# Performance work log

Measured on AMD Instinct MI355X. Metric: run time of the kernel, lower is better.

The kernel has to match this reference:

```python
import jax, jax.numpy as jnp
import numpy as np

N = 50000
NUM_USERS = 20000
E = 800000
IN_DIM = 256
OUT_DIM = 256
H = 8
DK = OUT_DIM // H


def setup_inputs() -> dict:
    key = jax.random.key(0)
    ks = jax.random.split(key, 16)
    inp = {
        "x": jax.random.normal(ks[0], (N, IN_DIM), dtype=jnp.float32),
        "row": jax.random.randint(ks[1], (E,), 0, N, dtype=jnp.int32),
        "col": jax.random.randint(ks[2], (E,), 0, N, dtype=jnp.int32),
        "relation_emb": jax.random.normal(ks[3], (OUT_DIM,), dtype=jnp.float32),
        "user_text_embs": jax.random.normal(ks[4], (NUM_USERS, IN_DIM), dtype=jnp.float32),
        "item_text_embs": jax.random.normal(ks[5], (N - NUM_USERS, IN_DIM), dtype=jnp.float32),
        "Wq": jax.random.normal(ks[6], (OUT_DIM, IN_DIM), dtype=jnp.float32) * 0.02,
        "bq": jnp.zeros((OUT_DIM,), dtype=jnp.float32),
        "Wk": jax.random.normal(ks[7], (OUT_DIM, IN_DIM), dtype=jnp.float32) * 0.02,
        "bk": jnp.zeros((OUT_DIM,), dtype=jnp.float32),
        "Wv": jax.random.normal(ks[8], (OUT_DIM, IN_DIM), dtype=jnp.float32) * 0.02,
        "bv": jnp.zeros((OUT_DIM,), dtype=jnp.float32),
        "Wo": jax.random.normal(ks[9], (OUT_DIM, OUT_DIM), dtype=jnp.float32) * 0.02,
        "bo": jnp.zeros((OUT_DIM,), dtype=jnp.float32),
    }
    return inp


def reference(x, row, col, relation_emb, user_text_embs, item_text_embs,
              Wq, bq, Wk, bk, Wv, bv, Wo, bo):
    # text_emb: users first, then items (matches torch zeros_like + slice assign)
    text_emb = jnp.concatenate([user_text_embs, item_text_embs], axis=0)  # [N, in_dim]

    Q = (text_emb @ Wq.T + bq).reshape(N, H, DK)
    K = (text_emb @ Wk.T + bk).reshape(N, H, DK)
    V = (x @ Wv.T + bv).reshape(N, H, DK)

    Q_ = Q[col]  # [E, H, DK]
    K_ = K[row]
    V_ = V[row]
    rel = relation_emb.reshape(1, H, DK)

    scores = jnp.sum(Q_ * (K_ + rel), axis=-1) / np.sqrt(DK).astype(np.float32)  # [E, H]

    # segment softmax over destination node (col)
    m = jax.ops.segment_max(scores, col, num_segments=N)          # [N, H]
    e = jnp.exp(scores - m[col])                                   # [E, H]
    denom = jax.ops.segment_sum(e, col, num_segments=N)           # [N, H]
    attn = e / denom[col]                                          # [E, H]

    out = jax.ops.segment_sum(attn[:, :, None] * V_, col, num_segments=N)  # [N, H, DK]
    out = out.reshape(N, OUT_DIM)
    return out @ Wo.T + bo
```

## Files before the change

kernel.cpp:

```cpp
#include <hip/hip_runtime.h>
#include <hip/hip_bf16.h>

#define N_NODES   50000
#define N_USERS   20000
#define N_EDGES   800000
#define DIM       256
#define NHEAD     8
#define DKH       32
#define NBLK_SCAN ((N_NODES + 255) / 256)
#define NGRP      (N_NODES / 16)
#define NGRP_PAD  3128
#define SLOTS_NODE (NGRP * 8 * 64)
#define NBLK_CAST (SLOTS_NODE / 256)
#define NBLK_HIST ((N_EDGES + 255) / 256)
#define NBLK_G64  (NGRP_PAD / 4)
#define KVROW     768

typedef __attribute__((ext_vector_type(8))) short bf16x8;
typedef __attribute__((ext_vector_type(4))) float f32x4;
typedef __attribute__((ext_vector_type(4))) unsigned short u16x4;
typedef __attribute__((ext_vector_type(8))) unsigned short u16x8;

__device__ inline unsigned short f2bf(float f) {
    union { __hip_bfloat16 b; unsigned short u; } cv;
    cv.b = __float2bfloat16(f);
    return cv.u;
}
__device__ inline float bf2f(unsigned short u) {
    return __uint_as_float(((unsigned int)u) << 16);
}
__device__ inline unsigned char f2fp8(float f) {
    unsigned int p = __builtin_amdgcn_cvt_pk_fp8_f32(f, f, 0, false);
    return (unsigned char)(p & 0xff);
}


__global__ void prep_kernel(const float* __restrict__ Wq, const float* __restrict__ Wk,
                            const float* __restrict__ Wv, const float* __restrict__ Wo,
                            unsigned short* __restrict__ Wb2,
                            const float* __restrict__ x,
                            const float* __restrict__ user, const float* __restrict__ item,
                            unsigned short* __restrict__ xb2, unsigned short* __restrict__ tb2,
                            const int* __restrict__ col, int* __restrict__ cnt,
                            int* __restrict__ erank)
{
    int b = blockIdx.x;
    if (b < 128) {
        int gid = b * 256 + threadIdx.x;
        const float* srcs[4] = { Wq, Wk, Wv, Wo };
        int m = gid >> 13, slot = gid & 8191;
        int lane = slot & 63, ks = (slot >> 6) & 7, g = slot >> 9;
        int c = g * 16 + (lane & 15);
        int d = ks * 32 + (lane >> 4) * 8;
        const float* s = srcs[m] + (size_t)c * DIM + d;
        float4 f0 = *(const float4*)s, f1 = *(const float4*)(s + 4);
        u16x8 o = { f2bf(f0.x), f2bf(f0.y), f2bf(f0.z), f2bf(f0.w),
                    f2bf(f1.x), f2bf(f1.y), f2bf(f1.z), f2bf(f1.w) };
        *(u16x8*)(Wb2 + (size_t)m * 65536 + (size_t)slot * 8) = o;
    } else if (b < 128 + NBLK_CAST) {
        int slot = (b - 128) * 256 + threadIdx.x;
        int lane = slot & 63, ks = (slot >> 6) & 7, g = slot >> 9;
        int r = g * 16 + (lane & 15);
        int d = ks * 32 + (lane >> 4) * 8;

        const float* sx = x + (size_t)r * DIM + d;
        float4 f0 = *(const float4*)sx, f1 = *(const float4*)(sx + 4);
        u16x8 xo = { f2bf(f0.x), f2bf(f0.y), f2bf(f0.z), f2bf(f0.w),
                     f2bf(f1.x), f2bf(f1.y), f2bf(f1.z), f2bf(f1.w) };
        *(u16x8*)(xb2 + (size_t)slot * 8) = xo;

        const float* st = (r < N_USERS) ? user + (size_t)r * DIM + d
                                        : item + (size_t)(r - N_USERS) * DIM + d;
        float4 t0 = *(const float4*)st, t1 = *(const float4*)(st + 4);
        u16x8 to = { f2bf(t0.x), f2bf(t0.y), f2bf(t0.z), f2bf(t0.w),
                     f2bf(t1.x), f2bf(t1.y), f2bf(t1.z), f2bf(t1.w) };
        *(u16x8*)(tb2 + (size_t)slot * 8) = to;
    } else {
        int e = (b - 128 - NBLK_CAST) * 256 + threadIdx.x;
        if (e < N_EDGES) erank[e] = atomicAdd(&cnt[col[e]], 1);
    }
}

__device__ __forceinline__ void mfma_core64(const unsigned short* __restrict__ A2,
                                            const unsigned short* __restrict__ W2,
                                            int row0, f32x4 acc[2][8],
                                            int lane, int wid)
{
    const int gA = (row0 >> 4) + (wid >> 1) * 2;
    const int gB = (wid & 1) * 8;
    #pragma unroll
    for (int ks = 0; ks < 8; ++ks) {
        bf16x8 a[2], b[8];
        #pragma unroll
        for (int i = 0; i < 2; ++i)
            a[i] = *(const bf16x8*)(A2 + (size_t)((gA + i) * 8 + ks) * 512 + lane * 8);
        #pragma unroll
        for (int j = 0; j < 8; ++j)
            b[j] = *(const bf16x8*)(W2 + (size_t)((gB + j) * 8 + ks) * 512 + lane * 8);
        #pragma unroll
        for (int i = 0; i < 2; ++i)
            #pragma unroll
            for (int j = 0; j < 8; ++j)
                acc[i][j] = __builtin_amdgcn_mfma_f32_16x16x32_bf16(a[i], b[j], acc[i][j], 0, 0, 0);
    }
}

template<int MODE>
__device__ __forceinline__ void epilogue64(f32x4 acc[2][8], const float* bias, void* Cv,
                                           int row0, int M, int lane, int wid)
{
    const int wm = wid >> 1, wn = wid & 1;
    const int lr = lane & 15, lk = lane >> 4;
    float* Cf = (float*)Cv;
    unsigned short* Cb = (unsigned short*)Cv;
    unsigned char* C8 = (unsigned char*)Cv;
    #pragma unroll
    for (int i = 0; i < 2; ++i) {
        #pragma unroll
        for (int r = 0; r < 4; ++r) {
            int grow = row0 + wm * 32 + i * 16 + lk * 4 + r;
            if (grow >= M) continue;
            #pragma unroll
            for (int j = 0; j < 8; ++j) {
                int gcol = wn * 128 + j * 16 + lr;
                float val = acc[i][j][r] + bias[gcol];
                if constexpr (MODE == 0) {
                    Cf[(size_t)grow * 256 + gcol] = val;
                } else if constexpr (MODE == 1) {
                    Cb[(size_t)grow * 256 + gcol] = f2bf(val);
                } else if constexpr (MODE == 2) {
                    C8[(size_t)grow * KVROW + gcol] = f2fp8(val);
                } else {
                    *(unsigned short*)(C8 + (size_t)grow * KVROW + 256 + gcol * 2) = f2bf(val);
                }
            }
        }
    }
}

__global__ __launch_bounds__(256) void gemm_qkv_scatter(
    const unsigned short* __restrict__ tb2, const unsigned short* __restrict__ xb2,
    const unsigned short* __restrict__ Wb2,
    const float* __restrict__ bq, const float* __restrict__ bk, const float* __restrict__ bv,
    unsigned short* __restrict__ Qb, unsigned char* __restrict__ KVb, int M,
    const int* __restrict__ row, const int* __restrict__ col,
    const int* __restrict__ erank, const int* __restrict__ offs,
    int* __restrict__ esrc)
{
    const int b = blockIdx.x;
    if (b < NBLK_HIST) {
        int e = b * 256 + threadIdx.x;
        if (e < N_EDGES) {
            int c = col[e];
            esrc[offs[c] + erank[e]] = row[e];
        }
        return;
    }
    const int gb = b - NBLK_HIST;
    const int mat = gb / NBLK_G64;
    const int row0 = (gb % NBLK_G64) * 64;
    const int tid = threadIdx.x;
    const int lane = tid & 63, wid = tid >> 6;

    const unsigned short* A2 = (mat == 2) ? xb2 : tb2;
    const unsigned short* W2 = Wb2 + (size_t)mat * 65536;

    f32x4 acc[2][8];
    #pragma unroll
    for (int i = 0; i < 2; ++i)
        #pragma unroll
        for (int j = 0; j < 8; ++j) acc[i][j] = (f32x4){0.f, 0.f, 0.f, 0.f};

    mfma_core64(A2, W2, row0, acc, lane, wid);

    if (mat == 0)      epilogue64<1>(acc, bq, Qb,  row0, M, lane, wid);
    else if (mat == 1) epilogue64<2>(acc, bk, KVb, row0, M, lane, wid);
    else               epilogue64<3>(acc, bv, KVb, row0, M, lane, wid);
}

__global__ __launch_bounds__(256) void gemm_o_reg(
    const unsigned short* __restrict__ A2,
    const unsigned short* __restrict__ Wb2, const float* __restrict__ bo,
    float* __restrict__ C, int M)
{
    const int tid = threadIdx.x;
    const int lane = tid & 63, wid = tid >> 6;
    const int row0 = blockIdx.x * 64;

    f32x4 acc[2][8];
    #pragma unroll
    for (int i = 0; i < 2; ++i)
        #pragma unroll
        for (int j = 0; j < 8; ++j) acc[i][j] = (f32x4){0.f, 0.f, 0.f, 0.f};

    mfma_core64(A2, Wb2 + 3 * 65536, row0, acc, lane, wid);
    epilogue64<0>(acc, bo, C, row0, M, lane, wid);
}

__global__ __launch_bounds__(256) void scan_blk_kernel(const int* __restrict__ cnt,
                                                       int* __restrict__ offs_tmp,
                                                       int* __restrict__ bsum) {
    __shared__ int s[256];
    int b = blockIdx.x, t = threadIdx.x;
    int i = b * 256 + t;
    int v = (i < N_NODES) ? cnt[i] : 0;
    s[t] = v;
    __syncthreads();
    #pragma unroll
    for (int d = 1; d < 256; d <<= 1) {
        int u = (t >= d) ? s[t - d] : 0;
        __syncthreads();
        s[t] += u;
        __syncthreads();
    }
    if (i < N_NODES) offs_tmp[i] = s[t] - v;
    if (t == 255) bsum[b] = s[255];
}

__global__ __launch_bounds__(256) void scan_top_kernel(int* __restrict__ bsum) {
    __shared__ int s[256];
    int t = threadIdx.x;
    int v = (t < NBLK_SCAN) ? bsum[t] : 0;
    s[t] = v;
    __syncthreads();
    #pragma unroll
    for (int d = 1; d < 256; d <<= 1) {
        int u = (t >= d) ? s[t - d] : 0;
        __syncthreads();
        s[t] += u;
        __syncthreads();
    }
    if (t < NBLK_SCAN) bsum[t] = s[t] - v;
}

__global__ __launch_bounds__(256) void scan_add_kernel(const int* __restrict__ offs_tmp,
                                                       const int* __restrict__ bsum,
                                                       int* __restrict__ offs) {
    int i = blockIdx.x * 256 + threadIdx.x;
    if (i == 0) offs[N_NODES] = N_EDGES;
    if (i >= N_NODES) return;
    offs[i] = offs_tmp[i] + bsum[blockIdx.x];
}

__global__ __launch_bounds__(256) void node_fused_kernel(
    const unsigned short* __restrict__ Qb, const unsigned char* __restrict__ KVb,
    const float* __restrict__ rel,
    const int* __restrict__ offs, const int* __restrict__ esrc,
    unsigned short* __restrict__ outagg2)
{
    const float SC = 0.17677669529663687f;
    int wid = (blockIdx.x * blockDim.x + threadIdx.x) >> 6;
    int lane = threadIdx.x & 63;
    if (wid >= N_NODES) return;
    int beg = offs[wid], end = offs[wid + 1];
    int d0 = lane * 4;
    const unsigned char* kbase = KVb + lane * 4;
    const unsigned char* vbase = KVb + 256 + lane * 8;

    u16x4 qb4 = *(const u16x4*)(Qb + (size_t)wid * DIM + d0);
    float qx = bf2f(qb4[0]), qy = bf2f(qb4[1]), qz = bf2f(qb4[2]), qw = bf2f(qb4[3]);
    float4 rl = *(const float4*)(rel + d0);

    float p0 = qx * rl.x + qy * rl.y + qz * rl.z + qw * rl.w;
    p0 += __shfl_xor(p0, 1);
    p0 += __shfl_xor(p0, 2);
    p0 += __shfl_xor(p0, 4);

    float den = 0.f;
    float4 acc = make_float4(0.f, 0.f, 0.f, 0.f);

    for (int base = beg; base < end; base += 64) {
        int n = end - base; if (n > 64) n = 64;
        int idx = base + lane; if (idx >= end) idx = end - 1;
        int my = esrc[idx];
        int j = 0;
        for (; j + 8 <= n; j += 8) {
            unsigned int kw[8]; u16x4 vv[8];
            #pragma unroll
            for (int u = 0; u < 8; ++u) {
                int r = __shfl(my, j + u);
                size_t ro = (size_t)r * KVROW;
                kw[u] = *(const unsigned int*)(kbase + ro);
                vv[u] = *(const u16x4*)(vbase + ro);
            }
            float s[8];
            #pragma unroll
            for (int u = 0; u < 8; ++u)
                s[u] = qx * __builtin_amdgcn_cvt_f32_fp8(kw[u], 0)
                     + qy * __builtin_amdgcn_cvt_f32_fp8(kw[u], 1)
                     + qz * __builtin_amdgcn_cvt_f32_fp8(kw[u], 2)
                     + qw * __builtin_amdgcn_cvt_f32_fp8(kw[u], 3);
            #pragma unroll
            for (int u = 0; u < 8; ++u) {
                s[u] += __shfl_xor(s[u], 1);
                s[u] += __shfl_xor(s[u], 2);
                s[u] += __shfl_xor(s[u], 4);
            }
            #pragma unroll
            for (int u = 0; u < 8; ++u) {
                float w = __expf((s[u] + p0) * SC);
                den += w;
                acc.x += w * bf2f(vv[u][0]); acc.y += w * bf2f(vv[u][1]);
                acc.z += w * bf2f(vv[u][2]); acc.w += w * bf2f(vv[u][3]);
            }
        }
        for (; j + 4 <= n; j += 4) {
            unsigned int kw[4]; u16x4 vv[4];
            #pragma unroll
            for (int u = 0; u < 4; ++u) {
                int r = __shfl(my, j + u);
                size_t ro = (size_t)r * KVROW;
                kw[u] = *(const unsigned int*)(kbase + ro);
                vv[u] = *(const u16x4*)(vbase + ro);
            }
            float s[4];
            #pragma unroll
            for (int u = 0; u < 4; ++u)
                s[u] = qx * __builtin_amdgcn_cvt_f32_fp8(kw[u], 0)
                     + qy * __builtin_amdgcn_cvt_f32_fp8(kw[u], 1)
                     + qz * __builtin_amdgcn_cvt_f32_fp8(kw[u], 2)
                     + qw * __builtin_amdgcn_cvt_f32_fp8(kw[u], 3);
            #pragma unroll
            for (int u = 0; u < 4; ++u) {
                s[u] += __shfl_xor(s[u], 1);
                s[u] += __shfl_xor(s[u], 2);
                s[u] += __shfl_xor(s[u], 4);
            }
            #pragma unroll
            for (int u = 0; u < 4; ++u) {
                float w = __expf((s[u] + p0) * SC);
                den += w;
                acc.x += w * bf2f(vv[u][0]); acc.y += w * bf2f(vv[u][1]);
                acc.z += w * bf2f(vv[u][2]); acc.w += w * bf2f(vv[u][3]);
            }
        }
        for (; j < n; ++j) {
            int r = __shfl(my, j);
            size_t ro = (size_t)r * KVROW;
            unsigned int kw = *(const unsigned int*)(kbase + ro);
            u16x4 vv = *(const u16x4*)(vbase + ro);
            float s0 = qx * __builtin_amdgcn_cvt_f32_fp8(kw, 0)
                     + qy * __builtin_amdgcn_cvt_f32_fp8(kw, 1)
                     + qz * __builtin_amdgcn_cvt_f32_fp8(kw, 2)
                     + qw * __builtin_amdgcn_cvt_f32_fp8(kw, 3);
            s0 += __shfl_xor(s0, 1);
            s0 += __shfl_xor(s0, 2);
            s0 += __shfl_xor(s0, 4);
            float w0 = __expf((s0 + p0) * SC);
            den += w0;
            acc.x += w0 * bf2f(vv[0]); acc.y += w0 * bf2f(vv[1]);
            acc.z += w0 * bf2f(vv[2]); acc.w += w0 * bf2f(vv[3]);
        }
    }
    float rden = (end > beg) ? 1.f / den : 0.f;
    u16x4 o = { f2bf(acc.x * rden), f2bf(acc.y * rden),
                f2bf(acc.z * rden), f2bf(acc.w * rden) };
    int ks = lane >> 3, lk = (lane >> 1) & 3, e4 = (lane & 1) * 4;
    size_t toff = ((size_t)(wid >> 4) * 8 + ks) * 512 + (lk * 16 + (wid & 15)) * 8 + e4;
    *(u16x4*)(outagg2 + toff) = o;
}

extern "C" void kernel_launch(void* const* d_in, const int* in_sizes, int n_in,
                              void* d_out, int out_size, void* d_ws, size_t ws_size,
                              hipStream_t stream) {
    const float* x    = (const float*)d_in[0];
    const int*   row  = (const int*)d_in[1];
    const int*   col  = (const int*)d_in[2];
    const float* rel  = (const float*)d_in[3];
    const float* user = (const float*)d_in[4];
    const float* item = (const float*)d_in[5];
    const float* Wq   = (const float*)d_in[6];
    const float* bq   = (const float*)d_in[7];
    const float* Wk   = (const float*)d_in[8];
    const float* bk   = (const float*)d_in[9];
    const float* Wv   = (const float*)d_in[10];
    const float* bv   = (const float*)d_in[11];
    const float* Wo   = (const float*)d_in[12];
    const float* bo   = (const float*)d_in[13];

    char* ws = (char*)d_ws;
    size_t off = 0;
    auto alloc = [&](size_t bytes) -> void* {
        void* p = ws + off;
        off = (off + bytes + 255) & ~(size_t)255;
        return p;
    };
    const size_t tiled_sz = (size_t)NGRP_PAD * 4096 * 2;
    unsigned short* Qb      = (unsigned short*)alloc((size_t)N_NODES * DIM * 2);
    unsigned char*  KVb     = (unsigned char*)alloc((size_t)N_NODES * KVROW);
    unsigned short* xb2     = (unsigned short*)alloc(tiled_sz);
    unsigned short* tb2     = (unsigned short*)alloc(tiled_sz);
    unsigned short* outagg2 = (unsigned short*)alloc(tiled_sz);
    unsigned short* Wb2     = (unsigned short*)alloc((size_t)4 * 65536 * 2);
    int*   cnt      = (int*)alloc((size_t)N_NODES * 4);
    int*   offs     = (int*)alloc((size_t)(N_NODES + 1) * 4);
    int*   offs_tmp = (int*)alloc((size_t)N_NODES * 4);
    int*   bsum     = (int*)alloc((size_t)NBLK_SCAN * 4);
    int*   esrc     = (int*)alloc((size_t)N_EDGES * 4);
    int*   erank    = (int*)alloc((size_t)N_EDGES * 4);

    hipMemsetAsync(cnt, 0, (size_t)N_NODES * 4, stream);

    prep_kernel<<<128 + NBLK_CAST + NBLK_HIST, 256, 0, stream>>>(
        Wq, Wk, Wv, Wo, Wb2, x, user, item, xb2, tb2, col, cnt, erank);
    scan_blk_kernel<<<NBLK_SCAN, 256, 0, stream>>>(cnt, offs_tmp, bsum);
    scan_top_kernel<<<1, 256, 0, stream>>>(bsum);
    scan_add_kernel<<<NBLK_SCAN, 256, 0, stream>>>(offs_tmp, bsum, offs);

    gemm_qkv_scatter<<<NBLK_HIST + 3 * NBLK_G64, 256, 0, stream>>>(
        tb2, xb2, Wb2, bq, bk, bv, Qb, KVb, N_NODES,
        row, col, erank, offs, esrc);

    node_fused_kernel<<<(N_NODES * 64 + 255) / 256, 256, 0, stream>>>(
        Qb, KVb, rel, offs, esrc, outagg2);

    gemm_o_reg<<<NBLK_G64, 256, 0, stream>>>(outagg2, Wb2, bo, (float*)d_out, N_NODES);
}
```

Measured before the change: 252.0 us.

## Fuse fp32-to-bf16 input cast into QKV GEMM via LDS staging and share tile for Q/K

Removes the separate pass that casts x and text embeddings into tiled bf16 buffers. The QKV GEMM blocks now load fp32 rows directly, convert them to bf16 and stage them in a 32KB LDS tile in MFMA layout. Q and K blocks share one staged text tile and run two GEMMs back to back, which cuts the block count from three to two per row group. The cost is less parallelism and more LDS use per block, plus uncoalesced-ish fp32 loads inside the GEMM.

```diff
diff --git a/kernel.cpp b/kernel.cpp
--- a/kernel.cpp
+++ b/kernel.cpp
@@ -8,10 +8,7 @@
 #define NHEAD     8
 #define DKH       32
 #define NBLK_SCAN ((N_NODES + 255) / 256)
-#define NGRP      (N_NODES / 16)
 #define NGRP_PAD  3128
-#define SLOTS_NODE (NGRP * 8 * 64)
-#define NBLK_CAST (SLOTS_NODE / 256)
 #define NBLK_HIST ((N_EDGES + 255) / 256)
 #define NBLK_G64  (NGRP_PAD / 4)
 #define KVROW     768
@@ -38,9 +35,6 @@
 __global__ void prep_kernel(const float* __restrict__ Wq, const float* __restrict__ Wk,
                             const float* __restrict__ Wv, const float* __restrict__ Wo,
                             unsigned short* __restrict__ Wb2,
-                            const float* __restrict__ x,
-                            const float* __restrict__ user, const float* __restrict__ item,
-                            unsigned short* __restrict__ xb2, unsigned short* __restrict__ tb2,
                             const int* __restrict__ col, int* __restrict__ cnt,
                             int* __restrict__ erank)
 {
@@ -57,27 +51,53 @@
         u16x8 o = { f2bf(f0.x), f2bf(f0.y), f2bf(f0.z), f2bf(f0.w),
                     f2bf(f1.x), f2bf(f1.y), f2bf(f1.z), f2bf(f1.w) };
         *(u16x8*)(Wb2 + (size_t)m * 65536 + (size_t)slot * 8) = o;
-    } else if (b < 128 + NBLK_CAST) {
-        int slot = (b - 128) * 256 + threadIdx.x;
-        int lane = slot & 63, ks = (slot >> 6) & 7, g = slot >> 9;
-        int r = g * 16 + (lane & 15);
-        int d = ks * 32 + (lane >> 4) * 8;
-
-        const float* sx = x + (size_t)r * DIM + d;
-        float4 f0 = *(const float4*)sx, f1 = *(const float4*)(sx + 4);
-        u16x8 xo = { f2bf(f0.x), f2bf(f0.y), f2bf(f0.z), f2bf(f0.w),
+    } else {
+        int e = (b - 128) * 256 + threadIdx.x;
+        if (e < N_EDGES) erank[e] = atomicAdd(&cnt[col[e]], 1);
+    }
+}
+
+__device__ __forceinline__ void stage_a_lds(const float* __restrict__ Alo,
+                                            const float* __restrict__ Ahi,
+                                            int split, int row0, int M,
+                                            unsigned short* Asm, int tid)
+{
+    const int d0 = (tid & 31) * 8;
+    const int rb = tid >> 5;
+    #pragma unroll
+    for (int it = 0; it < 8; ++it) {
+        int r = it * 8 + rb;
+        int ga = row0 + r; if (ga >= M) ga = M - 1;
+        const float* src = ((ga < split) ? Alo + (size_t)ga * DIM
+                                         : Ahi + (size_t)(ga - split) * DIM) + d0;
+        float4 f0 = *(const float4*)src, f1 = *(const float4*)(src + 4);
+        u16x8 hv = { f2bf(f0.x), f2bf(f0.y), f2bf(f0.z), f2bf(f0.w),
                      f2bf(f1.x), f2bf(f1.y), f2bf(f1.z), f2bf(f1.w) };
-        *(u16x8*)(xb2 + (size_t)slot * 8) = xo;
-
-        const float* st = (r < N_USERS) ? user + (size_t)r * DIM + d
-                                        : item + (size_t)(r - N_USERS) * DIM + d;
-        float4 t0 = *(const float4*)st, t1 = *(const float4*)(st + 4);
-        u16x8 to = { f2bf(t0.x), f2bf(t0.y), f2bf(t0.z), f2bf(t0.w),
-                     f2bf(t1.x), f2bf(t1.y), f2bf(t1.z), f2bf(t1.w) };
-        *(u16x8*)(tb2 + (size_t)slot * 8) = to;
-    } else {
-        int e = (b - 128 - NBLK_CAST) * 256 + threadIdx.x;
-        if (e < N_EDGES) erank[e] = atomicAdd(&cnt[col[e]], 1);
+        int g = r >> 4, ks = d0 >> 5, sub = (d0 >> 3) & 3;
+        *(u16x8*)((char*)Asm + (size_t)(g * 8 + ks) * 1024 + sub * 256 + (r & 15) * 16) = hv;
+    }
+}
+
+__device__ __forceinline__ void mfma_core_lds(const unsigned short* Asm,
+                                              const unsigned short* __restrict__ W2,
+                                              f32x4 acc[2][8], int lane, int wid)
+{
+    const int gAl = (wid >> 1) * 2;
+    const int gB = (wid & 1) * 8;
+    #pragma unroll
+    for (int ks = 0; ks < 8; ++ks) {
+        bf16x8 a[2], b[8];
+        #pragma unroll
+        for (int i = 0; i < 2; ++i)
+            a[i] = *(const bf16x8*)((const char*)Asm + (size_t)((gAl + i) * 8 + ks) * 1024 + lane * 16);
+        #pragma unroll
+        for (int j = 0; j < 8; ++j)
+            b[j] = *(const bf16x8*)(W2 + (size_t)((gB + j) * 8 + ks) * 512 + lane * 8);
+        #pragma unroll
+        for (int i = 0; i < 2; ++i)
+            #pragma unroll
+            for (int j = 0; j < 8; ++j)
+                acc[i][j] = __builtin_amdgcn_mfma_f32_16x16x32_bf16(a[i], b[j], acc[i][j], 0, 0, 0);
     }
 }
 
@@ -139,7 +159,8 @@
 }
 
 __global__ __launch_bounds__(256) void gemm_qkv_scatter(
-    const unsigned short* __restrict__ tb2, const unsigned short* __restrict__ xb2,
+    const float* __restrict__ user, const float* __restrict__ item,
+    const float* __restrict__ x,
     const unsigned short* __restrict__ Wb2,
     const float* __restrict__ bq, const float* __restrict__ bk, const float* __restrict__ bv,
     unsigned short* __restrict__ Qb, unsigned char* __restrict__ KVb, int M,
@@ -156,26 +177,39 @@
         }
         return;
     }
+    __shared__ unsigned short Asm[64 * 256];
     const int gb = b - NBLK_HIST;
-    const int mat = gb / NBLK_G64;
-    const int row0 = (gb % NBLK_G64) * 64;
+    const int isv = gb >= NBLK_G64;
+    const int row0 = (isv ? gb - NBLK_G64 : gb) * 64;
     const int tid = threadIdx.x;
     const int lane = tid & 63, wid = tid >> 6;
 
-    const unsigned short* A2 = (mat == 2) ? xb2 : tb2;
-    const unsigned short* W2 = Wb2 + (size_t)mat * 65536;
+    if (isv) stage_a_lds(x, x, M, row0, M, Asm, tid);
+    else     stage_a_lds(user, item, N_USERS, row0, M, Asm, tid);
+    __syncthreads();
 
     f32x4 acc[2][8];
-    #pragma unroll
-    for (int i = 0; i < 2; ++i)
-        #pragma unroll
-        for (int j = 0; j < 8; ++j) acc[i][j] = (f32x4){0.f, 0.f, 0.f, 0.f};
-
-    mfma_core64(A2, W2, row0, acc, lane, wid);
-
-    if (mat == 0)      epilogue64<1>(acc, bq, Qb,  row0, M, lane, wid);
-    else if (mat == 1) epilogue64<2>(acc, bk, KVb, row0, M, lane, wid);
-    else               epilogue64<3>(acc, bv, KVb, row0, M, lane, wid);
+    if (isv) {
+        #pragma unroll
+        for (int i = 0; i < 2; ++i)
+            #pragma unroll
+            for (int j = 0; j < 8; ++j) acc[i][j] = (f32x4){0.f, 0.f, 0.f, 0.f};
+        mfma_core_lds(Asm, Wb2 + 2 * 65536, acc, lane, wid);
+        epilogue64<3>(acc, bv, KVb, row0, M, lane, wid);
+    } else {
+        #pragma unroll
+        for (int i = 0; i < 2; ++i)
+            #pragma unroll
+            for (int j = 0; j < 8; ++j) acc[i][j] = (f32x4){0.f, 0.f, 0.f, 0.f};
+        mfma_core_lds(Asm, Wb2, acc, lane, wid);
+        epilogue64<1>(acc, bq, Qb, row0, M, lane, wid);
+        #pragma unroll
+        for (int i = 0; i < 2; ++i)
+            #pragma unroll
+            for (int j = 0; j < 8; ++j) acc[i][j] = (f32x4){0.f, 0.f, 0.f, 0.f};
+        mfma_core_lds(Asm, Wb2 + 65536, acc, lane, wid);
+        epilogue64<2>(acc, bk, KVb, row0, M, lane, wid);
+    }
 }
 
 __global__ __launch_bounds__(256) void gemm_o_reg(
@@ -388,8 +422,6 @@
     const size_t tiled_sz = (size_t)NGRP_PAD * 4096 * 2;
     unsigned short* Qb      = (unsigned short*)alloc((size_t)N_NODES * DIM * 2);
     unsigned char*  KVb     = (unsigned char*)alloc((size_t)N_NODES * KVROW);
-    unsigned short* xb2     = (unsigned short*)alloc(tiled_sz);
-    unsigned short* tb2     = (unsigned short*)alloc(tiled_sz);
     unsigned short* outagg2 = (unsigned short*)alloc(tiled_sz);
     unsigned short* Wb2     = (unsigned short*)alloc((size_t)4 * 65536 * 2);
     int*   cnt      = (int*)alloc((size_t)N_NODES * 4);
@@ -401,14 +433,14 @@
 
     hipMemsetAsync(cnt, 0, (size_t)N_NODES * 4, stream);
 
-    prep_kernel<<<128 + NBLK_CAST + NBLK_HIST, 256, 0, stream>>>(
-        Wq, Wk, Wv, Wo, Wb2, x, user, item, xb2, tb2, col, cnt, erank);
+    prep_kernel<<<128 + NBLK_HIST, 256, 0, stream>>>(
+        Wq, Wk, Wv, Wo, Wb2, col, cnt, erank);
     scan_blk_kernel<<<NBLK_SCAN, 256, 0, stream>>>(cnt, offs_tmp, bsum);
     scan_top_kernel<<<1, 256, 0, stream>>>(bsum);
     scan_add_kernel<<<NBLK_SCAN, 256, 0, stream>>>(offs_tmp, bsum, offs);
 
-    gemm_qkv_scatter<<<NBLK_HIST + 3 * NBLK_G64, 256, 0, stream>>>(
-        tb2, xb2, Wb2, bq, bk, bv, Qb, KVb, N_NODES,
+    gemm_qkv_scatter<<<NBLK_HIST + 2 * NBLK_G64, 256, 0, stream>>>(
+        user, item, x, Wb2, bq, bk, bv, Qb, KVb, N_NODES,
         row, col, erank, offs, esrc);
 
     node_fused_kernel<<<(N_NODES * 64 + 255) / 256, 256, 0, stream>>>(
```

Result: faster. 226.6 us (-10.1%).
